# Performance work log

Measured on AMD Instinct MI355X. Metric: run time of the kernel, lower is better.

## Reference

```python
import jax, jax.numpy as jnp
import numpy as np

DEPTH = 4
H1 = 64
H2 = 16
NF = 5
L = 10.0
K = 4
DIM = 3
N = 2048
NK = N // 4
FEAT = 1 + 2 * NF * DIM  # r scalar + Nf (cos,sin) pairs of dim components


def _tn(k, shape, std=0.01):
    return jax.random.truncated_normal(k, -2.0, 2.0, shape, jnp.float32) * std


def setup_inputs() -> dict:
    key = jax.random.key(0)
    ks = jax.random.split(key, 16)
    comb0 = 3 * DIM + 3 * FEAT   # combine width at depth 0
    combd = 3 * H1 + 3 * H2      # combine width at later depths
    return {
        "sx": jax.random.uniform(ks[0], (N, DIM), jnp.float32) * L,
        "kpoints": jax.random.normal(ks[1], (2 * NK, DIM), jnp.float32),
        "we0": _tn(ks[2], (comb0, H1)), "be0": jnp.zeros((H1,), jnp.float32),
        "we_rest": _tn(ks[3], (DEPTH - 1, combd, H1)), "be_rest": jnp.zeros((DEPTH - 1, H1), jnp.float32),
        "wee0": _tn(ks[4], (FEAT, H2)), "bee0": jnp.zeros((H2,), jnp.float32),
        "wee_rest": _tn(ks[5], (DEPTH - 2, H2, H2)), "bee_rest": jnp.zeros((DEPTH - 2, H2), jnp.float32),
        "wep0": _tn(ks[6], (FEAT, H2)), "bep0": jnp.zeros((H2,), jnp.float32),
        "wep_rest": _tn(ks[7], (DEPTH - 2, H2, H2)), "bep_rest": jnp.zeros((DEPTH - 2, H2), jnp.float32),
        "orb_w_re": _tn(ks[8], (H1, H1)), "orb_w_im": _tn(ks[9], (H1, H1)),
        "orb_b_re": jnp.zeros((H1,), jnp.float32), "orb_b_im": jnp.zeros((H1,), jnp.float32),
        "w_det": _tn(ks[10], (K, H1, H1)),
        "bf_w": _tn(ks[11], (H1, DIM)),
        "mlp_w1": _tn(ks[12], (DIM, H1)), "mlp_b1": jnp.zeros((H1,), jnp.float32),
        "mlp_w2": _tn(ks[13], (H1, K * (NK - 1))), "mlp_b2": jnp.zeros((K * (NK - 1),), jnp.float32),
    }


def _fourier(rij, r):
    # interleaved [r, cos1, sin1, ..., cosNf, sinNf] like the original
    feats = [r[..., None]]
    for k in range(1, NF + 1):
        ang = (2.0 * np.pi * k / L) * rij
        feats.append(jnp.cos(ang))
        feats.append(jnp.sin(ang))
    return jnp.concatenate(feats, axis=-1)


def _combine(e, ee, ep):
    mm = e.shape[0]
    h = mm // 2
    g1a = jnp.broadcast_to(jnp.mean(e[:h], 0, keepdims=True), e.shape)
    g1b = jnp.broadcast_to(jnp.mean(e[h:], 0, keepdims=True), e.shape)
    g2a = jnp.mean(ee[:h], axis=0)
    g2b = jnp.mean(ee[h:], axis=0)
    g3 = jnp.mean(ep, axis=1)
    return jnp.concatenate([e, g1a, g1b, g2a, g2b, g3], axis=1)


def _forward(sx, kpoints, we0, be0, we_rest, be_rest, wee0, bee0, wee_rest, bee_rest,
             wep0, bep0, wep_rest, bep_rest, orb_w_re, orb_w_im, orb_b_re, orb_b_im,
             w_det, bf_w, mlp_w1, mlp_b1, mlp_w2, mlp_b2):
    n, dim = sx.shape
    m, m2 = n // 2, n // 4
    s, x = sx[:m], sx[m:]
    e = jnp.broadcast_to(kpoints[0][None, :], (m, dim))
    # electron-electron pairwise features (m,m,FEAT)
    rij = x[:, None, :] - x[None, :, :]
    eye = jnp.eye(m, dtype=x.dtype)
    r = jnp.linalg.norm(jnp.sin(np.pi * rij / L) + eye[..., None], axis=-1) * (1.0 - eye) * (L / np.pi)
    ee = _fourier(rij, r)
    # electron-proton pairwise features (m,m,FEAT)
    rij = x[:, None, :] - s[None, :, :]
    r = jnp.linalg.norm(jnp.sin(np.pi * rij / L), axis=-1) * (L / np.pi)
    ep = _fourier(rij, r)
    for d in range(DEPTH - 1):
        f = _combine(e, ee, ep)
        We, be = (we0, be0) if d == 0 else (we_rest[d - 1], be_rest[d - 1])
        Wee, bee = (wee0, bee0) if d == 0 else (wee_rest[d - 1], bee_rest[d - 1])
        Wep, bep = (wep0, bep0) if d == 0 else (wep_rest[d - 1], bep_rest[d - 1])
        e_u = jnp.tanh(f @ We + be)
        ee_u = jnp.tanh(ee @ Wee + bee)
        ep_u = jnp.tanh(ep @ Wep + bep)
        e, ee, ep = (e_u + e, ee_u + ee, ep_u + ep) if d > 0 else (e_u, ee_u, ep_u)
    f = _combine(e, ee, ep)
    e = jnp.tanh(f @ we_rest[-1] + be_rest[-1]) + e
    # complex orbitals and geminal pairing matrix phi: (K, m2, m2)
    orb = e.astype(jnp.complex64) @ (orb_w_re + 1j * orb_w_im) + (orb_b_re + 1j * orb_b_im)
    phi = jnp.einsum('ia,kab,jb->kij', orb[:m2], w_det.astype(jnp.complex64), orb[m2:]) + 1.0
    # backflow coordinates and plane-wave determinant factors
    z = e @ bf_w + x
    nk = kpoints.shape[0] // 2
    norm = 1.0 / L ** (dim / 2)
    D_up = norm * jnp.exp(1j * jnp.einsum('kd,id->ki', kpoints[:nk], z[:m2]))  # (nk, m2)
    D_dn = norm * jnp.exp(1j * jnp.einsum('kd,id->ki', kpoints[nk:], z[m2:]))  # (nk, m2)
    h = jnp.tanh(kpoints[0] @ mlp_w1 + mlp_b1)
    fdet = jax.nn.softplus(h @ mlp_w2 + mlp_b2).reshape(K, nk - 1)
    fdet = jnp.concatenate([jnp.ones((K, 1), fdet.dtype), fdet], axis=1)  # (K, nk)
    D = jnp.einsum('ai,ka,aj->kij', D_up, fdet.astype(D_up.dtype), jnp.conj(D_dn))
    # logdet_matmul: stable log of signed sum of K determinants
    phase, logabs = jnp.linalg.slogdet(D * phi)
    maxl = jnp.max(logabs)
    det = jnp.sum(phase * jnp.exp(logabs - maxl))
    return jnp.log(jnp.abs(det)) + maxl + jnp.log(det / jnp.abs(det))


def reference(sx, kpoints, we0, be0, we_rest, be_rest, wee0, bee0, wee_rest, bee_rest,
              wep0, bep0, wep_rest, bep_rest, orb_w_re, orb_w_im, orb_b_re, orb_b_im,
              w_det, bf_w, mlp_w1, mlp_b1, mlp_w2, mlp_b2):
    return _forward(sx, kpoints, we0, be0, we_rest, be_rest, wee0, bee0, wee_rest, bee_rest,
                    wep0, bep0, wep_rest, bep_rest, orb_w_re, orb_w_im, orb_b_re, orb_b_im,
                    w_det, bf_w, mlp_w1, mlp_b1, mlp_w2, mlp_b2)
```

## Files before the change

kernel.cpp:

```cpp
#include <hip/hip_runtime.h>

typedef unsigned int uint;
typedef unsigned short ushort;

#define M1 1024
#define MH 512
#define PI_F 3.14159265358979323846f
#define LBOX 10.0f
#define NB 32

__device__ __forceinline__ float bf2f(ushort h){ return __uint_as_float(((uint)h)<<16); }
__device__ __forceinline__ ushort f2bf(float f){ uint u = __float_as_uint(f); uint r = (u + 0x7fffu + ((u>>16)&1u))>>16; return (ushort)r; }
__device__ __forceinline__ float ftanh(float x){ float e = __expf(2.f*x); return 1.f - 2.f/(e+1.f); }
__device__ __forceinline__ float2 cmul(float2 a, float2 b){ return make_float2(a.x*b.x - a.y*b.y, a.x*b.y + a.y*b.x); }
__device__ __forceinline__ void cfma(float2& c, float2 a, float2 b){
  c.x = fmaf(a.x,b.x,fmaf(-a.y,b.y,c.x));
  c.y = fmaf(a.x,b.y,fmaf(a.y,b.x,c.y));
}

__device__ __forceinline__ void fourier31(float d0, float d1, float d2, bool diag, float f[31]){
  const float k1 = PI_F / LBOX;
  float s[3], c[3];
  __sincosf(k1*d0, &s[0], &c[0]);
  __sincosf(k1*d1, &s[1], &c[1]);
  __sincosf(k1*d2, &s[2], &c[2]);
  float r = diag ? 0.f : (LBOX/PI_F)*sqrtf(s[0]*s[0]+s[1]*s[1]+s[2]*s[2]);
  f[0] = r;
  float cb[3], sb[3], cc[3], sc[3];
  #pragma unroll
  for (int d=0; d<3; ++d){ cb[d] = 1.f - 2.f*s[d]*s[d]; sb[d] = 2.f*s[d]*c[d]; cc[d]=cb[d]; sc[d]=sb[d]; }
  #pragma unroll
  for (int k=0;k<5;++k){
    #pragma unroll
    for (int d=0; d<3; ++d){ f[1+6*k+d] = cc[d]; f[4+6*k+d] = sc[d]; }
    if (k<4){
      #pragma unroll
      for (int d=0; d<3; ++d){
        float nc = cc[d]*cb[d]-sc[d]*sb[d];
        float ns = sc[d]*cb[d]+cc[d]*sb[d];
        cc[d]=nc; sc[d]=ns;
      }
    }
  }
}

__global__ void k_init(float* __restrict__ p, int n, int* __restrict__ rowmap){
  int i = blockIdx.x*256 + threadIdx.x;
  if (i < 2048) rowmap[i] = i & 511;
  for (int q=i; q<n; q+=gridDim.x*256) p[q] = 0.f;
}

__global__ __launch_bounds__(256) void k_pair0(const float* __restrict__ sx, const float* __restrict__ W,
                                               const float* __restrict__ b, ushort* __restrict__ out, int is_ee,
                                               float* __restrict__ gA, float* __restrict__ gB,
                                               float* __restrict__ gH){
  int bx = blockIdx.x;
  int i = bx >> 2;
  int chunk = bx & 3;
  int j = (chunk << 8) + threadIdx.x;
  const float* xs = sx + 3*M1;
  float xi0 = xs[3*i], xi1 = xs[3*i+1], xi2 = xs[3*i+2];
  const float* oth = is_ee ? xs : sx;
  float y0 = oth[3*j], y1 = oth[3*j+1], y2 = oth[3*j+2];
  float f[31];
  fourier31(xi0-y0, xi1-y1, xi2-y2, is_ee && (i==j), f);
  float acc[16];
  #pragma unroll
  for (int o=0;o<16;++o) acc[o] = b[o];
  #pragma unroll
  for (int c=0;c<31;++c){ float fv = f[c];
    #pragma unroll
    for (int o=0;o<16;++o) acc[o] = fmaf(fv, W[c*16+o], acc[o]);
  }
  float hv[16];
  #pragma unroll
  for (int o=0;o<16;++o) hv[o] = ftanh(acc[o]);
  uint u[8];
  #pragma unroll
  for (int h=0;h<8;++h){
    u[h] = (uint)f2bf(hv[2*h]) | ((uint)f2bf(hv[2*h+1])<<16);
  }
  uint4* dst = (uint4*)(out + ((size_t)i*M1 + j)*16);
  dst[0] = make_uint4(u[0],u[1],u[2],u[3]);
  dst[1] = make_uint4(u[4],u[5],u[6],u[7]);
  __shared__ float buf[256*49];
  #pragma unroll
  for (int c=0;c<31;++c) buf[threadIdx.x*49+c] = f[c];
  #pragma unroll
  for (int c=0;c<16;++c) buf[threadIdx.x*49+31+c] = hv[c];
  __syncthreads();
  #pragma unroll
  for (int s=128; s>0; s>>=1){
    if (threadIdx.x < s){
      #pragma unroll
      for (int c=0;c<47;++c) buf[threadIdx.x*49+c] += buf[(threadIdx.x+s)*49+c];
    }
    __syncthreads();
  }
  if (threadIdx.x < 31){
    float* g = (is_ee && chunk >= 2) ? gB : gA;
    atomicAdd(&g[i*31+threadIdx.x], buf[threadIdx.x]);
  } else if (threadIdx.x < 47 && gH){
    atomicAdd(&gH[i*16 + (threadIdx.x-31)], buf[threadIdx.x]);
  }
}

__global__ __launch_bounds__(256) void k_pairU(ushort* __restrict__ ten, const float* __restrict__ W,
                                               const float* __restrict__ b, float* __restrict__ gOut){
  size_t base = ((size_t)blockIdx.x*256 + threadIdx.x)*16;
  uint4 a0 = ((uint4*)(ten+base))[0];
  uint4 a1 = ((uint4*)(ten+base))[1];
  uint uu[8] = {a0.x,a0.y,a0.z,a0.w,a1.x,a1.y,a1.z,a1.w};
  float v[16];
  #pragma unroll
  for (int h=0;h<8;++h){ v[2*h] = bf2f((ushort)(uu[h]&0xffffu)); v[2*h+1] = bf2f((ushort)(uu[h]>>16)); }
  float acc[16];
  #pragma unroll
  for (int o=0;o<16;++o) acc[o] = b[o];
  #pragma unroll
  for (int c=0;c<16;++c){ float fv = v[c];
    #pragma unroll
    for (int o=0;o<16;++o) acc[o] = fmaf(fv, W[c*16+o], acc[o]);
  }
  float nv[16];
  #pragma unroll
  for (int o=0;o<16;++o) nv[o] = ftanh(acc[o]) + v[o];
  uint w[8];
  #pragma unroll
  for (int h=0;h<8;++h){
    w[h] = (uint)f2bf(nv[2*h]) | ((uint)f2bf(nv[2*h+1])<<16);
  }
  ((uint4*)(ten+base))[0] = make_uint4(w[0],w[1],w[2],w[3]);
  ((uint4*)(ten+base))[1] = make_uint4(w[4],w[5],w[6],w[7]);
  __shared__ float buf[256*17];
  if (gOut){
    #pragma unroll
    for (int c=0;c<16;++c) buf[threadIdx.x*17+c] = nv[c];
    __syncthreads();
    #pragma unroll
    for (int s=128; s>0; s>>=1){
      if (threadIdx.x < s){
        #pragma unroll
        for (int c=0;c<16;++c) buf[threadIdx.x*17+c] += buf[(threadIdx.x+s)*17+c];
      }
      __syncthreads();
    }
    if (threadIdx.x < 16){
      int i = blockIdx.x >> 2;
      atomicAdd(&gOut[i*16 + threadIdx.x], buf[threadIdx.x]);
    }
  }
}

__global__ __launch_bounds__(256) void k_gee(const ushort* __restrict__ ten, float* __restrict__ gA, float* __restrict__ gB){
  int jb = blockIdx.x >> 3;
  int ic = blockIdx.x & 7;
  int jl = threadIdx.x & 63;
  int iq = threadIdx.x >> 6;
  int j = jb*64 + jl;
  float acc[16];
  #pragma unroll
  for (int c=0;c<16;++c) acc[c]=0.f;
  for (int s=0;s<32;++s){
    int i = ic*128 + iq + 4*s;
    const uint4* src = (const uint4*)(ten + ((size_t)i*M1 + j)*16);
    uint4 a0 = src[0], a1 = src[1];
    uint uu[8]={a0.x,a0.y,a0.z,a0.w,a1.x,a1.y,a1.z,a1.w};
    #pragma unroll
    for (int h=0;h<8;++h){ acc[2*h]+=bf2f((ushort)(uu[h]&0xffffu)); acc[2*h+1]+=bf2f((ushort)(uu[h]>>16)); }
  }
  __shared__ float red[4][64][16];
  #pragma unroll
  for (int c=0;c<16;++c) red[iq][jl][c]=acc[c];
  __syncthreads();
  if (iq==0){
    float* out = (ic<4)? gA : gB;
    #pragma unroll
    for (int c=0;c<16;++c){
      float t = red[0][jl][c]+red[1][jl][c]+red[2][jl][c]+red[3][jl][c];
      atomicAdd(&out[j*16+c], t);
    }
  }
}

__global__ __launch_bounds__(256) void k_e0(const float* __restrict__ kp, const float* __restrict__ g2a,
    const float* __restrict__ g2b, const float* __restrict__ g3, const float* __restrict__ W,
    const float* __restrict__ b, float* __restrict__ eout, float* __restrict__ g1out){
  int p = blockIdx.x*4 + (threadIdx.x>>6);
  int o = threadIdx.x & 63;
  float acc = b[o];
  #pragma unroll
  for (int d=0; d<3; ++d){
    acc = fmaf(kp[d], W[d*64+o] + W[(d+3)*64+o] + W[(d+6)*64+o], acc);
  }
  const float i512 = 1.f/512.f, i1024 = 1.f/1024.f;
  #pragma unroll
  for (int c=0;c<31;++c){
    float sg = (c!=0 && ((c-1)%6)>=3) ? -i512 : i512;
    acc = fmaf(g2a[p*31+c]*sg, W[(9+c)*64+o], acc);
  }
  #pragma unroll
  for (int c=0;c<31;++c){
    float sg = (c!=0 && ((c-1)%6)>=3) ? -i512 : i512;
    acc = fmaf(g2b[p*31+c]*sg, W[(40+c)*64+o], acc);
  }
  #pragma unroll
  for (int c=0;c<31;++c) acc = fmaf(g3[p*31+c]*i1024, W[(71+c)*64+o], acc);
  float v = ftanh(acc);
  eout[p*64+o] = v;
  atomicAdd(&g1out[(p<MH?0:64)+o], v);
}

__global__ __launch_bounds__(256) void k_eupd(const float* __restrict__ eprev, float* __restrict__ eout,
    const float* __restrict__ W, const float* __restrict__ b, const float* __restrict__ g1in,
    const float* __restrict__ g2a, const float* __restrict__ g2b, const float* __restrict__ g3,
    float* __restrict__ g1out){
  int p = blockIdx.x*4 + (threadIdx.x>>6);
  int o = threadIdx.x & 63;
  const float i512 = 1.f/512.f, i1024 = 1.f/1024.f;
  float acc = b[o];
  #pragma unroll 8
  for (int c=0;c<64;++c) acc = fmaf(eprev[p*64+c], W[c*64+o], acc);
  #pragma unroll 8
  for (int c=0;c<64;++c) acc = fmaf(g1in[c]*i512, W[(64+c)*64+o], acc);
  #pragma unroll 8
  for (int c=0;c<64;++c) acc = fmaf(g1in[64+c]*i512, W[(128+c)*64+o], acc);
  #pragma unroll
  for (int c=0;c<16;++c) acc = fmaf(g2a[p*16+c]*i512, W[(192+c)*64+o], acc);
  #pragma unroll
  for (int c=0;c<16;++c) acc = fmaf(g2b[p*16+c]*i512, W[(208+c)*64+o], acc);
  #pragma unroll
  for (int c=0;c<16;++c) acc = fmaf(g3[p*16+c]*i1024, W[(224+c)*64+o], acc);
  float v = ftanh(acc) + eprev[p*64+o];
  eout[p*64+o] = v;
  if (g1out) atomicAdd(&g1out[(p<MH?0:64)+o], v);
}

__global__ __launch_bounds__(256) void k_orbz(const float* __restrict__ e4, const float* __restrict__ Wre,
    const float* __restrict__ Wim, const float* __restrict__ bre, const float* __restrict__ bim,
    const float* __restrict__ bfw, const float* __restrict__ sx, float* __restrict__ ore,
    float* __restrict__ oim, float* __restrict__ z){
  int p = blockIdx.x*4 + (threadIdx.x>>6);
  int o = threadIdx.x & 63;
  float ar = bre[o], ai = bim[o];
  #pragma unroll 8
  for (int a=0;a<64;++a){ float ev = e4[p*64+a]; ar = fmaf(ev, Wre[a*64+o], ar); ai = fmaf(ev, Wim[a*64+o], ai); }
  ore[p*64+o]=ar; oim[p*64+o]=ai;
  if (o<3){
    float zz = sx[(M1+p)*3+o];
    for (int a=0;a<64;++a) zz = fmaf(e4[p*64+a], bfw[a*3+o], zz);
    z[p*3+o]=zz;
  }
}

__global__ __launch_bounds__(256) void k_fdet(const float* __restrict__ kp, const float* __restrict__ w1,
    const float* __restrict__ b1, const float* __restrict__ w2, const float* __restrict__ b2,
    float* __restrict__ fdet){
  __shared__ float hs[64];
  int tid = threadIdx.x;
  if (tid < 64){
    float acc = b1[tid];
    for (int d=0;d<3;++d) acc = fmaf(kp[d], w1[d*64+tid], acc);
    hs[tid] = ftanh(acc);
  }
  __syncthreads();
  int c = blockIdx.x*256 + tid;
  if (c < 2044){
    float acc = b2[c];
    #pragma unroll 8
    for (int o=0;o<64;++o) acc = fmaf(hs[o], w2[o*2044+c], acc);
    float sp = (acc > 20.f) ? acc : log1pf(__expf(acc));
    int kk = c / 511, idx = c % 511;
    fdet[kk*512 + 1 + idx] = sp;
  }
  if (blockIdx.x == 0 && tid < 4) fdet[tid*512] = 1.f;
}

__global__ __launch_bounds__(256) void k_uv(const float* __restrict__ kp, const float* __restrict__ z,
                                            float2* __restrict__ U, float2* __restrict__ V){
  int gid = blockIdx.x*256 + threadIdx.x;
  int sel = gid >> 18;
  int rem = gid & 262143;
  int a = rem >> 9;
  int col = rem & 511;
  const float nrm = 0.031622776601683794f;
  const float* kr = kp + (sel ? (512+a)*3 : a*3);
  const float* zr = z + (sel ? (512+col)*3 : col*3);
  float th = kr[0]*zr[0] + kr[1]*zr[1] + kr[2]*zr[2];
  float s, c; __sincosf(th, &s, &c);
  float2 v = make_float2(nrm*c, nrm*s);
  if (sel) V[a*512+col] = v; else U[a*512+col] = v;
}

__global__ __launch_bounds__(256) void k_T(const float* __restrict__ ore, const float* __restrict__ oim,
                                           const float* __restrict__ wdet, float2* __restrict__ T){
  int k = blockIdx.x >> 7;
  int iblk = blockIdx.x & 127;
  int i = iblk*4 + (threadIdx.x>>6);
  int bc = threadIdx.x & 63;
  __shared__ float wd[4096];
  for (int t = threadIdx.x; t < 4096; t += 256) wd[t] = wdet[k*4096 + t];
  __syncthreads();
  float ar=0.f, ai=0.f;
  #pragma unroll 8
  for (int a=0;a<64;++a){
    float w = wd[a*64+bc];
    ar = fmaf(ore[i*64+a], w, ar);
    ai = fmaf(oim[i*64+a], w, ai);
  }
  T[((size_t)k*512 + i)*64 + bc] = make_float2(ar, ai);
}

__global__ __launch_bounds__(256) void k_M(const float2* __restrict__ U, const float2* __restrict__ V,
    const float* __restrict__ fdet, const float2* __restrict__ T, const float* __restrict__ ore,
    const float* __restrict__ oim, float2* __restrict__ Mb){
  __shared__ float2 sm[4160];
  int k = blockIdx.x >> 8;
  int ty = (blockIdx.x >> 4) & 15;
  int tx = blockIdx.x & 15;
  int ib = ty*32, jb = tx*32;
  int i0 = (threadIdx.x >> 4)*2;
  int j0 = threadIdx.x & 15;
  const float* fk = fdet + k*512;
  float2 a00={0,0},a01={0,0},a10={0,0},a11={0,0};
  float2* As = sm;
  float2* Bs = sm + 512;
  for (int a0=0; a0<512; a0+=16){
    for (int t = threadIdx.x; t < 512; t += 256){
      int aa = t >> 5, il = t & 31;
      int a = a0 + aa;
      float fv = fk[a];
      float2 u = U[a*512 + ib + il];
      As[t] = make_float2(u.x*fv, u.y*fv);
      float2 v = V[a*512 + jb + il];
      Bs[t] = make_float2(v.x, -v.y);
    }
    __syncthreads();
    #pragma unroll
    for (int aa=0; aa<16; ++aa){
      float2 A0 = As[aa*32+i0], A1 = As[aa*32+i0+1];
      float2 B0 = Bs[aa*32+j0], B1 = Bs[aa*32+j0+16];
      cfma(a00,A0,B0); cfma(a01,A0,B1); cfma(a10,A1,B0); cfma(a11,A1,B1);
    }
    __syncthreads();
  }
  float2* Ts = sm;
  float2* Od = sm + 2080;
  for (int t = threadIdx.x; t < 2048; t += 256){
    int il = t >> 6, bc = t & 63;
    Ts[il*65+bc] = T[((size_t)k*512 + ib + il)*64 + bc];
    int oidx = (512 + jb + il)*64 + bc;
    Od[il*65+bc] = make_float2(ore[oidx], oim[oidx]);
  }
  __syncthreads();
  float2 p00={1,0},p01={1,0},p10={1,0},p11={1,0};
  #pragma unroll 8
  for (int bb=0; bb<64; ++bb){
    float2 T0 = Ts[i0*65+bb], T1 = Ts[(i0+1)*65+bb];
    float2 O0 = Od[j0*65+bb], O1 = Od[(j0+16)*65+bb];
    cfma(p00,T0,O0); cfma(p01,T0,O1); cfma(p10,T1,O0); cfma(p11,T1,O1);
  }
  size_t base = ((size_t)k*512 + ib + i0)*512 + jb;
  Mb[base+j0]        = cmul(a00, p00);
  Mb[base+j0+16]     = cmul(a01, p01);
  Mb[base+512+j0]    = cmul(a10, p10);
  Mb[base+512+j0+16] = cmul(a11, p11);
}

__global__ __launch_bounds__(512)
void k_panel(float2* __restrict__ Mb, float2* __restrict__ LinvG,
             int* __restrict__ rowmap, int* __restrict__ swapc, int col0){
  int k = blockIdx.x;
  float2* Mk = Mb + (size_t)k*512*512;
  int R = 512 - col0;
  int R64 = R < 64 ? R : 64;
  int rl = threadIdx.x;
  bool active = rl < R;
  int wv = rl >> 6;
  __shared__ float2 mir[64*33];
  __shared__ float2 Us[NB*33];
  __shared__ float2 dinv[NB];
  __shared__ float2 Ls[NB*NB];
  __shared__ float2 Yv[NB*NB];
  __shared__ int winslot[NB];
  __shared__ int newposS[64];
  int rm_orig = active ? rowmap[k*512 + col0 + rl] : 0;
  float2 X[NB];
  if (rl >= 64 && active){
    const float4* rp = (const float4*)(Mk + (size_t)rm_orig*512 + col0);
    #pragma unroll
    for (int q=0;q<NB/2;++q){ float4 v = rp[q]; X[2*q]=make_float2(v.x,v.y); X[2*q+1]=make_float2(v.z,v.w); }
  }
  if (wv == 0){
    if (rl < R64){
      const float4* rp = (const float4*)(Mk + (size_t)rm_orig*512 + col0);
      #pragma unroll
      for (int q=0;q<NB/2;++q){
        float4 v = rp[q];
        mir[rl*33+2*q]   = make_float2(v.x,v.y);
        mir[rl*33+2*q+1] = make_float2(v.z,v.w);
      }
    }
    bool done = false;
    int winpos = 0;
    for (int cc=0; cc<NB; ++cc){
      bool cand = (rl < R64) && !done;
      float2 cv = make_float2(0.f,0.f);
      if (cand) cv = mir[rl*33+cc];
      float val = cand ? fmaf(cv.x,cv.x,cv.y*cv.y) : -1.f;
      int idx = rl;
      #pragma unroll
      for (int off=32; off>0; off>>=1){
        float ov = __shfl_xor(val, off);
        int   oi = __shfl_xor(idx, off);
        if (ov > val || (ov == val && oi < idx)){ val = ov; idx = oi; }
      }
      int p = idx;
      if (rl == 0) winslot[cc] = p;
      if (rl == p){ done = true; winpos = cc; }
      float2 dg = mir[p*33+cc];
      float dn = 1.f/fmaf(dg.x,dg.x,dg.y*dg.y);
      float2 inv = make_float2(dg.x*dn, -dg.y*dn);
      if (cand && rl != p){
        float2 l = cmul(cv, inv);
        mir[rl*33+cc] = l;
        for (int j=cc+1; j<NB; ++j){
          float2 pr = mir[p*33+j];
          float2 xv = mir[rl*33+j];
          xv.x = fmaf(-l.x, pr.x, fmaf( l.y, pr.y, xv.x));
          xv.y = fmaf(-l.x, pr.y, fmaf(-l.y, pr.x, xv.y));
          mir[rl*33+j] = xv;
        }
      }
    }
    unsigned long long nwmask = __ballot(rl < R64 && !done);
    int np = 0;
    if (rl < R64){
      np = done ? winpos : (NB + (int)__popcll(nwmask & ((1ull<<rl)-1ull)));
      newposS[rl] = np;
      rowmap[k*512 + col0 + np] = rm_orig;
      float4* wp = (float4*)(Mk + (size_t)rm_orig*512 + col0);
      #pragma unroll
      for (int q=0;q<NB/2;++q){
        float2 a = mir[rl*33+2*q], bq = mir[rl*33+2*q+1];
        wp[q] = make_float4(a.x,a.y,bq.x,bq.y);
      }
    }
    {
      int cnt = 0;
      for (int t=0;t<R64;++t){
        int nt = newposS[t];
        if (rl < R64 && t > rl && nt < np) cnt++;
      }
      #pragma unroll
      for (int off=32; off>0; off>>=1) cnt += __shfl_xor(cnt, off);
      if (rl == 0) swapc[k] += cnt;
    }
    if (rl < NB){
      int ws = winslot[rl];
      #pragma unroll
      for (int j=0;j<NB;++j){
        float2 v = mir[ws*33+j];
        Us[rl*33+j] = v;
        float2 lv;
        if      (j <  rl) lv = v;
        else if (j == rl) lv = make_float2(1.f,0.f);
        else              lv = make_float2(0.f,0.f);
        Ls[rl*NB+j] = lv;
      }
      float2 d = Us[rl*33+rl];
      float dn = 1.f/fmaf(d.x,d.x,d.y*d.y);
      dinv[rl] = make_float2(d.x*dn, -d.y*dn);
    }
  }
  __syncthreads();
  if (rl >= 64 && active){
    #pragma unroll
    for (int j=0;j<NB;++j){
      float2 t = X[j];
      #pragma unroll
      for (int q=0;q<NB;++q){
        if (q < j){
          float2 u = Us[q*33+j];
          t.x = fmaf(-X[q].x, u.x, fmaf( X[q].y, u.y, t.x));
          t.y = fmaf(-X[q].x, u.y, fmaf(-X[q].y, u.x, t.y));
        }
      }
      X[j] = cmul(t, dinv[j]);
    }
    float4* wp = (float4*)(Mk + (size_t)rm_orig*512 + col0);
    #pragma unroll
    for (int q=0;q<NB/2;++q) wp[q] = make_float4(X[2*q].x,X[2*q].y,X[2*q+1].x,X[2*q+1].y);
  }
  if (rl < NB){
    for (int i=0;i<NB;++i){
      float2 acc = (i==rl)? make_float2(1.f,0.f) : make_float2(0.f,0.f);
      for (int q=rl; q<i; ++q){
        float2 lv = Ls[i*NB+q];
        float2 yv = Yv[q*NB+rl];
        acc.x = fmaf(-lv.x, yv.x, fmaf( lv.y, yv.y, acc.x));
        acc.y = fmaf(-lv.x, yv.y, fmaf(-lv.y, yv.x, acc.y));
      }
      Yv[i*NB+rl] = acc;
    }
  }
  __syncthreads();
  {
    float4* dst = (float4*)(LinvG + (size_t)k*(NB*NB));
    const float4* src = (const float4*)Yv;
    for (int q=rl; q<NB*NB/2; q+=blockDim.x) dst[q] = src[q];
  }
}

__global__ __launch_bounds__(256) void k_gemm(float2* __restrict__ Mb, const float2* __restrict__ LinvG,
                                              const int* __restrict__ rowmap, int col0){
  int k = blockIdx.z;
  float2* Mk = Mb + (size_t)k*512*512;
  int e0 = col0 + NB;
  int r0 = e0 + blockIdx.x*32;
  int j0c = e0 + blockIdx.y*32;
  int tid = threadIdx.x;
  int jl = tid & 31, rg = tid >> 5;
  __shared__ float2 As[NB*33];
  __shared__ float2 Bs[NB*33];
  __shared__ float2 Av[NB*33];
  __shared__ float2 Li[NB*NB];
  __shared__ int prA[32];
  __shared__ int prB[NB];
  if (tid < 32) prA[tid] = rowmap[k*512 + r0 + tid];
  else if (tid < 64) prB[tid-32] = rowmap[k*512 + col0 + (tid-32)];
  {
    const float4* src = (const float4*)(LinvG + (size_t)k*(NB*NB));
    float4* dst = (float4*)Li;
    for (int q=tid; q<NB*NB/2; q+=256) dst[q] = src[q];
  }
  __syncthreads();
  #pragma unroll
  for (int s=0;s<4;++s){
    int a = rg + 8*s;
    Av[a*33 + jl] = Mk[(size_t)prB[a]*512 + j0c + jl];
  }
  for (int t=tid; t<1024; t+=256){
    int rl = t >> 5, kk = t & 31;
    As[kk*33+rl] = Mk[(size_t)prA[rl]*512 + col0 + kk];
  }
  __syncthreads();
  #pragma unroll
  for (int s=0;s<4;++s){
    int m = rg + 8*s;
    float2 acc = make_float2(0.f,0.f);
    #pragma unroll 8
    for (int a=0;a<NB;++a) cfma(acc, Li[m*NB+a], Av[a*33+jl]);
    Bs[m*33+jl] = acc;
  }
  __syncthreads();
  int i0 = (tid >> 4)*2, j0 = (tid & 15)*2;
  float2 a00={0,0},a01={0,0},a10={0,0},a11={0,0};
  #pragma unroll 16
  for (int kk=0;kk<NB;++kk){
    float2 A0 = As[kk*33+i0], A1 = As[kk*33+i0+1];
    float2 B0 = Bs[kk*33+j0], B1 = Bs[kk*33+j0+1];
    cfma(a00,A0,B0); cfma(a01,A0,B1); cfma(a10,A1,B0); cfma(a11,A1,B1);
  }
  size_t ro0 = (size_t)prA[i0]*512 + j0c + j0;
  size_t ro1 = (size_t)prA[i0+1]*512 + j0c + j0;
  float2 c0 = Mk[ro0];   c0.x-=a00.x; c0.y-=a00.y; Mk[ro0]=c0;
  float2 c1 = Mk[ro0+1]; c1.x-=a01.x; c1.y-=a01.y; Mk[ro0+1]=c1;
  float2 c2 = Mk[ro1];   c2.x-=a10.x; c2.y-=a10.y; Mk[ro1]=c2;
  float2 c3 = Mk[ro1+1]; c3.x-=a11.x; c3.y-=a11.y; Mk[ro1+1]=c3;
}

__global__ void k_det(const float2* __restrict__ Mb, const int* __restrict__ rowmap,
                      const int* __restrict__ swapc, float* __restrict__ out, int out_size){
  int tid = threadIdx.x;
  int k = tid >> 6, lane = tid & 63;
  const float2* Mk = Mb + (size_t)k*512*512;
  double la = 0.0, ang = 0.0;
  for (int q=0;q<8;++q){
    int i = lane*8 + q;
    int pr = rowmap[k*512 + i];
    float2 u = Mk[(size_t)pr*512+i];
    double re = (double)u.x, im = (double)u.y;
    la += 0.5*log(re*re + im*im);
    ang += atan2(im, re);
  }
  #pragma unroll
  for (int off=32; off>0; off>>=1){
    la += __shfl_down(la, off);
    ang += __shfl_down(ang, off);
  }
  __shared__ double las[4], angs[4];
  if (lane==0){
    las[k] = la;
    angs[k] = ang + 3.14159265358979323846*(double)(swapc[k] & 1);
  }
  __syncthreads();
  if (tid==0){
    double mx = las[0];
    for (int q=1;q<4;++q) mx = fmax(mx, las[q]);
    double sre=0.0, sim=0.0;
    for (int q=0;q<4;++q){
      double w = exp(las[q]-mx);
      sre += w*cos(angs[q]);
      sim += w*sin(angs[q]);
    }
    double mag = sqrt(sre*sre+sim*sim);
    out[0] = (float)(log(mag)+mx);
    if (out_size > 1) out[1] = (float)atan2(sim, sre);
    for (int q=2;q<out_size;++q) out[q] = 0.f;
  }
}

extern "C" void kernel_launch(void* const* d_in, const int* in_sizes, int n_in,
                              void* d_out, int out_size, void* d_ws, size_t ws_size,
                              hipStream_t stream){
  const float* sx   = (const float*)d_in[0];
  const float* kp   = (const float*)d_in[1];
  const float* we0  = (const float*)d_in[2];
  const float* be0  = (const float*)d_in[3];
  const float* weR  = (const float*)d_in[4];
  const float* beR  = (const float*)d_in[5];
  const float* wee0 = (const float*)d_in[6];
  const float* bee0 = (const float*)d_in[7];
  const float* weeR = (const float*)d_in[8];
  const float* beeR = (const float*)d_in[9];
  const float* wep0 = (const float*)d_in[10];
  const float* bep0 = (const float*)d_in[11];
  const float* wepR = (const float*)d_in[12];
  const float* bepR = (const float*)d_in[13];
  const float* owre = (const float*)d_in[14];
  const float* owim = (const float*)d_in[15];
  const float* obre = (const float*)d_in[16];
  const float* obim = (const float*)d_in[17];
  const float* wdet = (const float*)d_in[18];
  const float* bfw  = (const float*)d_in[19];
  const float* mw1  = (const float*)d_in[20];
  const float* mb1  = (const float*)d_in[21];
  const float* mw2  = (const float*)d_in[22];
  const float* mb2  = (const float*)d_in[23];

  char* ws = (char*)d_ws;
  size_t off = 0;
  auto alloc = [&](size_t bytes)->char*{
    char* p = ws + off;
    off = (off + bytes + 255) & ~(size_t)255;
    return p;
  };
  ushort* ee   = (ushort*)alloc(33554432);
  ushort* ep   = (ushort*)alloc(33554432);
  float2* Mb   = (float2*)alloc(8388608);
  float2* U    = (float2*)alloc(2097152);
  float2* V    = (float2*)alloc(2097152);
  float2* T    = (float2*)alloc(1048576);
  float*  eS   = (float*)alloc(1048576);
  float*  ore  = (float*)alloc(262144);
  float*  oim  = (float*)alloc(262144);
  float*  z    = (float*)alloc(12288);
  float*  fdet = (float*)alloc(8192);
  float2* Linv = (float2*)alloc(131072);
  int*    rowmap = (int*)alloc(8192);
  char*   zst  = ws + off;
  float*  g2a0 = (float*)alloc(126976);
  float*  g2b0 = (float*)alloc(126976);
  float*  g30  = (float*)alloc(126976);
  float*  geeA = (float*)alloc(196608);
  float*  geeB = (float*)alloc(196608);
  float*  gep  = (float*)alloc(196608);
  float*  g1s  = (float*)alloc(1536);
  int*    swpc = (int*)alloc(16);
  int zn = (int)(((char*)(swpc+4) - zst)/4);

  float* e1 = eS;           float* e2 = eS + 65536;
  float* e3 = eS + 131072;  float* e4 = eS + 196608;
  float* geeA1 = geeA;      float* geeA2 = geeA+16384; float* geeA3 = geeA+32768;
  float* geeB1 = geeB;      float* geeB2 = geeB+16384; float* geeB3 = geeB+32768;
  float* gep1  = gep;       float* gep2  = gep+16384;  float* gep3  = gep+32768;
  float* g1s1 = g1s; float* g1s2 = g1s+128; float* g1s3 = g1s+256;

  k_init<<<256,256,0,stream>>>((float*)zst, zn, rowmap);
  k_pair0<<<4096,256,0,stream>>>(sx, wee0, bee0, ee, 1, g2a0, g2b0, nullptr);
  k_pair0<<<4096,256,0,stream>>>(sx, wep0, bep0, ep, 0, g30, g30, gep1);
  k_e0<<<256,256,0,stream>>>(kp, g2a0, g2b0, g30, we0, be0, e1, g1s1);
  k_gee<<<128,256,0,stream>>>(ee, geeA1, geeB1);
  k_eupd<<<256,256,0,stream>>>(e1, e2, weR, beR, g1s1, geeA1, geeB1, gep1, g1s2);
  k_pairU<<<4096,256,0,stream>>>(ee, weeR, beeR, nullptr);
  k_pairU<<<4096,256,0,stream>>>(ep, wepR, bepR, gep2);
  k_gee<<<128,256,0,stream>>>(ee, geeA2, geeB2);
  k_eupd<<<256,256,0,stream>>>(e2, e3, weR+240*64, beR+64, g1s2, geeA2, geeB2, gep2, g1s3);
  k_pairU<<<4096,256,0,stream>>>(ee, weeR+256, beeR+16, nullptr);
  k_pairU<<<4096,256,0,stream>>>(ep, wepR+256, bepR+16, gep3);
  k_gee<<<128,256,0,stream>>>(ee, geeA3, geeB3);
  k_eupd<<<256,256,0,stream>>>(e3, e4, weR+2*240*64, beR+128, g1s3, geeA3, geeB3, gep3, nullptr);
  k_orbz<<<256,256,0,stream>>>(e4, owre, owim, obre, obim, bfw, sx, ore, oim, z);
  k_fdet<<<8,256,0,stream>>>(kp, mw1, mb1, mw2, mb2, fdet);
  k_uv<<<2048,256,0,stream>>>(kp, z, U, V);
  k_T<<<512,256,0,stream>>>(ore, oim, wdet, T);
  k_M<<<1024,256,0,stream>>>(U, V, fdet, T, ore, oim, Mb);
  for (int tpan=0;tpan<16;++tpan){
    int col0 = tpan*NB;
    int R = 512 - col0;
    int Rpad = (R + 63) & ~63;
    k_panel<<<4, Rpad, 0, stream>>>(Mb, Linv, rowmap, swpc, col0);
    if (tpan < 15){
      int nch = 15 - tpan;
      k_gemm<<<dim3(nch,nch,4),256,0,stream>>>(Mb, Linv, rowmap, col0);
    }
  }
  k_det<<<1,256,0,stream>>>(Mb, rowmap, swpc, (float*)d_out, out_size);
  (void)in_sizes; (void)n_in; (void)ws_size;
}
```

Baseline: 1.852 ms.

## Fuse electron-proton pair stream into one kernel and merge small tail kernels

The electron-proton pair features are only consumed through their per-electron means, so all three depth layers are now computed in registers inside one kernel. This removes the 32MB bf16 ep tensor and its two read-modify-write passes. The ee kernel is specialised and its hidden-state reduction dropped, since that path passed a null output. The separate fdet, U/V and T kernels are merged into one launch to cut launch overhead. The ep path now stays in fp32 instead of rounding to bf16 between layers, which slightly changes numerics, and the fused kernel runs two block reductions, which raises its register and shared-memory pressure.

```diff
diff --git a/kernel.cpp b/kernel.cpp
--- a/kernel.cpp
+++ b/kernel.cpp
@@ -50,20 +50,18 @@
   for (int q=i; q<n; q+=gridDim.x*256) p[q] = 0.f;
 }
 
-__global__ __launch_bounds__(256) void k_pair0(const float* __restrict__ sx, const float* __restrict__ W,
-                                               const float* __restrict__ b, ushort* __restrict__ out, int is_ee,
-                                               float* __restrict__ gA, float* __restrict__ gB,
-                                               float* __restrict__ gH){
+__global__ __launch_bounds__(256) void k_pair0ee(const float* __restrict__ sx, const float* __restrict__ W,
+                                                 const float* __restrict__ b, ushort* __restrict__ out,
+                                                 float* __restrict__ g2a, float* __restrict__ g2b){
   int bx = blockIdx.x;
   int i = bx >> 2;
   int chunk = bx & 3;
   int j = (chunk << 8) + threadIdx.x;
   const float* xs = sx + 3*M1;
   float xi0 = xs[3*i], xi1 = xs[3*i+1], xi2 = xs[3*i+2];
-  const float* oth = is_ee ? xs : sx;
-  float y0 = oth[3*j], y1 = oth[3*j+1], y2 = oth[3*j+2];
+  float y0 = xs[3*j], y1 = xs[3*j+1], y2 = xs[3*j+2];
   float f[31];
-  fourier31(xi0-y0, xi1-y1, xi2-y2, is_ee && (i==j), f);
+  fourier31(xi0-y0, xi1-y1, xi2-y2, (i==j), f);
   float acc[16];
   #pragma unroll
   for (int o=0;o<16;++o) acc[o] = b[o];
@@ -72,41 +70,114 @@
     #pragma unroll
     for (int o=0;o<16;++o) acc[o] = fmaf(fv, W[c*16+o], acc[o]);
   }
-  float hv[16];
-  #pragma unroll
-  for (int o=0;o<16;++o) hv[o] = ftanh(acc[o]);
   uint u[8];
   #pragma unroll
   for (int h=0;h<8;++h){
-    u[h] = (uint)f2bf(hv[2*h]) | ((uint)f2bf(hv[2*h+1])<<16);
+    ushort lo = f2bf(ftanh(acc[2*h]));
+    ushort hi = f2bf(ftanh(acc[2*h+1]));
+    u[h] = (uint)lo | ((uint)hi<<16);
   }
   uint4* dst = (uint4*)(out + ((size_t)i*M1 + j)*16);
   dst[0] = make_uint4(u[0],u[1],u[2],u[3]);
   dst[1] = make_uint4(u[4],u[5],u[6],u[7]);
-  __shared__ float buf[256*49];
-  #pragma unroll
-  for (int c=0;c<31;++c) buf[threadIdx.x*49+c] = f[c];
-  #pragma unroll
-  for (int c=0;c<16;++c) buf[threadIdx.x*49+31+c] = hv[c];
+  __shared__ float buf[256*33];
+  #pragma unroll
+  for (int c=0;c<31;++c) buf[threadIdx.x*33+c] = f[c];
   __syncthreads();
   #pragma unroll
   for (int s=128; s>0; s>>=1){
     if (threadIdx.x < s){
       #pragma unroll
+      for (int c=0;c<31;++c) buf[threadIdx.x*33+c] += buf[(threadIdx.x+s)*33+c];
+    }
+    __syncthreads();
+  }
+  if (threadIdx.x < 31){
+    float* g = (chunk >= 2) ? g2b : g2a;
+    atomicAdd(&g[i*31+threadIdx.x], buf[threadIdx.x]);
+  }
+}
+
+__global__ __launch_bounds__(256) void k_pair0ep(const float* __restrict__ sx,
+    const float* __restrict__ W0, const float* __restrict__ b0,
+    const float* __restrict__ W1, const float* __restrict__ b1,
+    const float* __restrict__ W2, const float* __restrict__ b2,
+    float* __restrict__ g3, float* __restrict__ gep1, float* __restrict__ gep2,
+    float* __restrict__ gep3){
+  int bx = blockIdx.x;
+  int i = bx >> 2;
+  int chunk = bx & 3;
+  int j = (chunk << 8) + threadIdx.x;
+  const float* xs = sx + 3*M1;
+  float xi0 = xs[3*i], xi1 = xs[3*i+1], xi2 = xs[3*i+2];
+  float y0 = sx[3*j], y1 = sx[3*j+1], y2 = sx[3*j+2];
+  float f[31];
+  fourier31(xi0-y0, xi1-y1, xi2-y2, false, f);
+  float acc[16];
+  #pragma unroll
+  for (int o=0;o<16;++o) acc[o] = b0[o];
+  #pragma unroll
+  for (int c=0;c<31;++c){ float fv = f[c];
+    #pragma unroll
+    for (int o=0;o<16;++o) acc[o] = fmaf(fv, W0[c*16+o], acc[o]);
+  }
+  float hv[16];
+  #pragma unroll
+  for (int o=0;o<16;++o) hv[o] = ftanh(acc[o]);
+  __shared__ float buf[256*49];
+  #pragma unroll
+  for (int c=0;c<31;++c) buf[threadIdx.x*49+c] = f[c];
+  #pragma unroll
+  for (int c=0;c<16;++c) buf[threadIdx.x*49+31+c] = hv[c];
+  __syncthreads();
+  #pragma unroll
+  for (int s=128; s>0; s>>=1){
+    if (threadIdx.x < s){
+      #pragma unroll
       for (int c=0;c<47;++c) buf[threadIdx.x*49+c] += buf[(threadIdx.x+s)*49+c];
     }
     __syncthreads();
   }
-  if (threadIdx.x < 31){
-    float* g = (is_ee && chunk >= 2) ? gB : gA;
-    atomicAdd(&g[i*31+threadIdx.x], buf[threadIdx.x]);
-  } else if (threadIdx.x < 47 && gH){
-    atomicAdd(&gH[i*16 + (threadIdx.x-31)], buf[threadIdx.x]);
-  }
+  if (threadIdx.x < 31) atomicAdd(&g3[i*31+threadIdx.x], buf[threadIdx.x]);
+  else if (threadIdx.x < 47) atomicAdd(&gep1[i*16 + (threadIdx.x-31)], buf[threadIdx.x]);
+  float v1[16];
+  #pragma unroll
+  for (int o=0;o<16;++o) acc[o] = b1[o];
+  #pragma unroll
+  for (int c=0;c<16;++c){ float fv = hv[c];
+    #pragma unroll
+    for (int o=0;o<16;++o) acc[o] = fmaf(fv, W1[c*16+o], acc[o]);
+  }
+  #pragma unroll
+  for (int o=0;o<16;++o) v1[o] = ftanh(acc[o]) + hv[o];
+  float v2[16];
+  #pragma unroll
+  for (int o=0;o<16;++o) acc[o] = b2[o];
+  #pragma unroll
+  for (int c=0;c<16;++c){ float fv = v1[c];
+    #pragma unroll
+    for (int o=0;o<16;++o) acc[o] = fmaf(fv, W2[c*16+o], acc[o]);
+  }
+  #pragma unroll
+  for (int o=0;o<16;++o) v2[o] = ftanh(acc[o]) + v1[o];
+  __syncthreads();
+  #pragma unroll
+  for (int c=0;c<16;++c){ buf[threadIdx.x*49+c] = v1[c]; buf[threadIdx.x*49+16+c] = v2[c]; }
+  __syncthreads();
+  #pragma unroll
+  for (int s=128; s>0; s>>=1){
+    if (threadIdx.x < s){
+      #pragma unroll
+      for (int c=0;c<32;++c) buf[threadIdx.x*49+c] += buf[(threadIdx.x+s)*49+c];
+    }
+    __syncthreads();
+  }
+  if (threadIdx.x < 16) atomicAdd(&gep2[i*16+threadIdx.x], buf[threadIdx.x]);
+  else if (threadIdx.x < 32) atomicAdd(&gep3[i*16+(threadIdx.x-16)], buf[threadIdx.x]);
 }
 
 __global__ __launch_bounds__(256) void k_pairU(ushort* __restrict__ ten, const float* __restrict__ W,
-                                               const float* __restrict__ b, float* __restrict__ gOut){
+                                               const float* __restrict__ b){
   size_t base = ((size_t)blockIdx.x*256 + threadIdx.x)*16;
   uint4 a0 = ((uint4*)(ten+base))[0];
   uint4 a1 = ((uint4*)(ten+base))[1];
@@ -122,34 +193,15 @@
     #pragma unroll
     for (int o=0;o<16;++o) acc[o] = fmaf(fv, W[c*16+o], acc[o]);
   }
-  float nv[16];
-  #pragma unroll
-  for (int o=0;o<16;++o) nv[o] = ftanh(acc[o]) + v[o];
   uint w[8];
   #pragma unroll
   for (int h=0;h<8;++h){
-    w[h] = (uint)f2bf(nv[2*h]) | ((uint)f2bf(nv[2*h+1])<<16);
+    float q0 = ftanh(acc[2*h]) + v[2*h];
+    float q1 = ftanh(acc[2*h+1]) + v[2*h+1];
+    w[h] = (uint)f2bf(q0) | ((uint)f2bf(q1)<<16);
   }
   ((uint4*)(ten+base))[0] = make_uint4(w[0],w[1],w[2],w[3]);
   ((uint4*)(ten+base))[1] = make_uint4(w[4],w[5],w[6],w[7]);
-  __shared__ float buf[256*17];
-  if (gOut){
-    #pragma unroll
-    for (int c=0;c<16;++c) buf[threadIdx.x*17+c] = nv[c];
-    __syncthreads();
-    #pragma unroll
-    for (int s=128; s>0; s>>=1){
-      if (threadIdx.x < s){
-        #pragma unroll
-        for (int c=0;c<16;++c) buf[threadIdx.x*17+c] += buf[(threadIdx.x+s)*17+c];
-      }
-      __syncthreads();
-    }
-    if (threadIdx.x < 16){
-      int i = blockIdx.x >> 2;
-      atomicAdd(&gOut[i*16 + threadIdx.x], buf[threadIdx.x]);
-    }
-  }
 }
 
 __global__ __launch_bounds__(256) void k_gee(const ushort* __restrict__ ten, float* __restrict__ gA, float* __restrict__ gB){
@@ -253,62 +305,62 @@
   }
 }
 
-__global__ __launch_bounds__(256) void k_fdet(const float* __restrict__ kp, const float* __restrict__ w1,
-    const float* __restrict__ b1, const float* __restrict__ w2, const float* __restrict__ b2,
-    float* __restrict__ fdet){
-  __shared__ float hs[64];
+__global__ __launch_bounds__(256) void k_uvTf(const float* __restrict__ kp, const float* __restrict__ z,
+    const float* __restrict__ ore, const float* __restrict__ oim, const float* __restrict__ wdet,
+    const float* __restrict__ w1, const float* __restrict__ b1, const float* __restrict__ w2,
+    const float* __restrict__ b2, float2* __restrict__ U, float2* __restrict__ V,
+    float2* __restrict__ T, float* __restrict__ fdet){
+  __shared__ float sh[4096];
+  int bx = blockIdx.x;
   int tid = threadIdx.x;
-  if (tid < 64){
-    float acc = b1[tid];
-    for (int d=0;d<3;++d) acc = fmaf(kp[d], w1[d*64+tid], acc);
-    hs[tid] = ftanh(acc);
-  }
-  __syncthreads();
-  int c = blockIdx.x*256 + tid;
-  if (c < 2044){
-    float acc = b2[c];
+  if (bx < 2048){
+    int gid = bx*256 + tid;
+    int sel = gid >> 18;
+    int rem = gid & 262143;
+    int a = rem >> 9;
+    int col = rem & 511;
+    const float nrm = 0.031622776601683794f;
+    const float* kr = kp + (sel ? (512+a)*3 : a*3);
+    const float* zr = z + (sel ? (512+col)*3 : col*3);
+    float th = kr[0]*zr[0] + kr[1]*zr[1] + kr[2]*zr[2];
+    float s, c; __sincosf(th, &s, &c);
+    float2 v = make_float2(nrm*c, nrm*s);
+    if (sel) V[a*512+col] = v; else U[a*512+col] = v;
+  } else if (bx < 2560){
+    int bb = bx - 2048;
+    int k = bb >> 7;
+    int iblk = bb & 127;
+    int i = iblk*4 + (tid>>6);
+    int bc = tid & 63;
+    for (int t = tid; t < 4096; t += 256) sh[t] = wdet[k*4096 + t];
+    __syncthreads();
+    float ar=0.f, ai=0.f;
     #pragma unroll 8
-    for (int o=0;o<64;++o) acc = fmaf(hs[o], w2[o*2044+c], acc);
-    float sp = (acc > 20.f) ? acc : log1pf(__expf(acc));
-    int kk = c / 511, idx = c % 511;
-    fdet[kk*512 + 1 + idx] = sp;
-  }
-  if (blockIdx.x == 0 && tid < 4) fdet[tid*512] = 1.f;
-}
-
-__global__ __launch_bounds__(256) void k_uv(const float* __restrict__ kp, const float* __restrict__ z,
-                                            float2* __restrict__ U, float2* __restrict__ V){
-  int gid = blockIdx.x*256 + threadIdx.x;
-  int sel = gid >> 18;
-  int rem = gid & 262143;
-  int a = rem >> 9;
-  int col = rem & 511;
-  const float nrm = 0.031622776601683794f;
-  const float* kr = kp + (sel ? (512+a)*3 : a*3);
-  const float* zr = z + (sel ? (512+col)*3 : col*3);
-  float th = kr[0]*zr[0] + kr[1]*zr[1] + kr[2]*zr[2];
-  float s, c; __sincosf(th, &s, &c);
-  float2 v = make_float2(nrm*c, nrm*s);
-  if (sel) V[a*512+col] = v; else U[a*512+col] = v;
-}
-
-__global__ __launch_bounds__(256) void k_T(const float* __restrict__ ore, const float* __restrict__ oim,
-                                           const float* __restrict__ wdet, float2* __restrict__ T){
-  int k = blockIdx.x >> 7;
-  int iblk = blockIdx.x & 127;
-  int i = iblk*4 + (threadIdx.x>>6);
-  int bc = threadIdx.x & 63;
-  __shared__ float wd[4096];
-  for (int t = threadIdx.x; t < 4096; t += 256) wd[t] = wdet[k*4096 + t];
-  __syncthreads();
-  float ar=0.f, ai=0.f;
-  #pragma unroll 8
-  for (int a=0;a<64;++a){
-    float w = wd[a*64+bc];
-    ar = fmaf(ore[i*64+a], w, ar);
-    ai = fmaf(oim[i*64+a], w, ai);
-  }
-  T[((size_t)k*512 + i)*64 + bc] = make_float2(ar, ai);
+    for (int a=0;a<64;++a){
+      float w = sh[a*64+bc];
+      ar = fmaf(ore[i*64+a], w, ar);
+      ai = fmaf(oim[i*64+a], w, ai);
+    }
+    T[((size_t)k*512 + i)*64 + bc] = make_float2(ar, ai);
+  } else {
+    int bb = bx - 2560;
+    if (tid < 64){
+      float acc = b1[tid];
+      for (int d=0;d<3;++d) acc = fmaf(kp[d], w1[d*64+tid], acc);
+      sh[tid] = ftanh(acc);
+    }
+    __syncthreads();
+    int c = bb*256 + tid;
+    if (c < 2044){
+      float acc = b2[c];
+      #pragma unroll 8
+      for (int o=0;o<64;++o) acc = fmaf(sh[o], w2[o*2044+c], acc);
+      float sp = (acc > 20.f) ? acc : log1pf(__expf(acc));
+      int kk = c / 511, idx = c % 511;
+      fdet[kk*512 + 1 + idx] = sp;
+    }
+    if (bb == 0 && tid < 4) fdet[tid*512] = 1.f;
+  }
 }
 
 __global__ __launch_bounds__(256) void k_M(const float2* __restrict__ U, const float2* __restrict__ V,
@@ -647,7 +699,6 @@
     return p;
   };
   ushort* ee   = (ushort*)alloc(33554432);
-  ushort* ep   = (ushort*)alloc(33554432);
   float2* Mb   = (float2*)alloc(8388608);
   float2* U    = (float2*)alloc(2097152);
   float2* V    = (float2*)alloc(2097152);
@@ -678,23 +729,20 @@
   float* g1s1 = g1s; float* g1s2 = g1s+128; float* g1s3 = g1s+256;
 
   k_init<<<256,256,0,stream>>>((float*)zst, zn, rowmap);
-  k_pair0<<<4096,256,0,stream>>>(sx, wee0, bee0, ee, 1, g2a0, g2b0, nullptr);
-  k_pair0<<<4096,256,0,stream>>>(sx, wep0, bep0, ep, 0, g30, g30, gep1);
+  k_pair0ee<<<4096,256,0,stream>>>(sx, wee0, bee0, ee, g2a0, g2b0);
+  k_pair0ep<<<4096,256,0,stream>>>(sx, wep0, bep0, wepR, bepR, wepR+256, bepR+16,
+                                   g30, gep1, gep2, gep3);
   k_e0<<<256,256,0,stream>>>(kp, g2a0, g2b0, g30, we0, be0, e1, g1s1);
   k_gee<<<128,256,0,stream>>>(ee, geeA1, geeB1);
   k_eupd<<<256,256,0,stream>>>(e1, e2, weR, beR, g1s1, geeA1, geeB1, gep1, g1s2);
-  k_pairU<<<4096,256,0,stream>>>(ee, weeR, beeR, nullptr);
-  k_pairU<<<4096,256,0,stream>>>(ep, wepR, bepR, gep2);
+  k_pairU<<<4096,256,0,stream>>>(ee, weeR, beeR);
   k_gee<<<128,256,0,stream>>>(ee, geeA2, geeB2);
   k_eupd<<<256,256,0,stream>>>(e2, e3, weR+240*64, beR+64, g1s2, geeA2, geeB2, gep2, g1s3);
-  k_pairU<<<4096,256,0,stream>>>(ee, weeR+256, beeR+16, nullptr);
-  k_pairU<<<4096,256,0,stream>>>(ep, wepR+256, bepR+16, gep3);
+  k_pairU<<<4096,256,0,stream>>>(ee, weeR+256, beeR+16);
   k_gee<<<128,256,0,stream>>>(ee, geeA3, geeB3);
   k_eupd<<<256,256,0,stream>>>(e3, e4, weR+2*240*64, beR+128, g1s3, geeA3, geeB3, gep3, nullptr);
   k_orbz<<<256,256,0,stream>>>(e4, owre, owim, obre, obim, bfw, sx, ore, oim, z);
-  k_fdet<<<8,256,0,stream>>>(kp, mw1, mb1, mw2, mb2, fdet);
-  k_uv<<<2048,256,0,stream>>>(kp, z, U, V);
-  k_T<<<512,256,0,stream>>>(ore, oim, wdet, T);
+  k_uvTf<<<2568,256,0,stream>>>(kp, z, ore, oim, wdet, mw1, mb1, mw2, mb2, U, V, T, fdet);
   k_M<<<1024,256,0,stream>>>(U, V, fdet, T, ore, oim, Mb);
   for (int tpan=0;tpan<16;++tpan){
     int col0 = tpan*NB;
```

Result: no change. 1.844 ms (-0.5%).
